# Kernel optimization log

Hardware: AMD Instinct MI355X
Metric: run time of the kernel (lower is better)

Reference implementation:

```python
import jax, jax.numpy as jnp
import numpy as np

B, T, N, H = 512, 128, 256, 256  # batch, time_step, input_size, hidden_size


def setup_inputs() -> dict:
    key = jax.random.key(0)
    ks = jax.random.split(key, 8)
    s_lin = 1.0 / np.sqrt(T)
    s_ih = 1.0 / np.sqrt(H)
    return {
        "X": jax.random.normal(ks[0], (B, T, N), dtype=jnp.float32),
        "Wq": jax.random.uniform(ks[1], (T, T), jnp.float32, -s_lin, s_lin),
        "Wk": jax.random.uniform(ks[2], (T, T), jnp.float32, -s_lin, s_lin),
        "Wv": jax.random.uniform(ks[3], (T, T), jnp.float32, -s_lin, s_lin),
        "W_ih": jax.random.uniform(ks[4], (4 * H, N), jnp.float32, -s_ih, s_ih),
        "W_hh": jax.random.uniform(ks[5], (4 * H, H), jnp.float32, -s_ih, s_ih),
        "b_ih": jax.random.uniform(ks[6], (4 * H,), jnp.float32, -s_ih, s_ih),
        "b_hh": jax.random.uniform(ks[7], (4 * H,), jnp.float32, -s_ih, s_ih),
    }


def _forward(X, Wq, Wk, Wv, W_ih, W_hh, b_ih, b_hh):
    b, t, n = X.shape
    Xp = jnp.swapaxes(X, 1, 2)  # (B, N, T)
    Q = Xp @ Wq.T               # (B, N, T)
    K = Xp @ Wk.T               # (B, N, T)
    V = Xp @ Wv.T               # (B, N, T)
    # QK[b,i,j] = sum_t Q[b,i,t] * K[b,j,t]; scale by sqrt(N)
    scores = jnp.einsum('bit,bjt->bij', Q, K) / jnp.sqrt(jnp.float32(n))
    A = jax.nn.softmax(scores, axis=-1)          # (B, N, N)
    Xa = jnp.einsum('bij,bjt->bit', A, V)        # (B, N, T)
    Xa = jnp.swapaxes(Xa, 1, 2)                  # (B, T, N)

    h0 = jnp.zeros((b, W_hh.shape[1]), X.dtype)
    c0 = h0

    def step(carry, x_t):
        h, c = carry
        gates = x_t @ W_ih.T + b_ih + h @ W_hh.T + b_hh  # (B, 4H)
        i, f, g, o = jnp.split(gates, 4, axis=-1)         # PyTorch gate order
        i = jax.nn.sigmoid(i)
        f = jax.nn.sigmoid(f)
        g = jnp.tanh(g)
        o = jax.nn.sigmoid(o)
        c = f * c + i * g
        h = o * jnp.tanh(c)
        return (h, c), h

    _, hs = jax.lax.scan(step, (h0, c0), jnp.swapaxes(Xa, 0, 1))  # (T, B, H)
    return jnp.swapaxes(hs, 0, 1)  # (B, T, H)


def reference(X, Wq, Wk, Wv, W_ih, W_hh, b_ih, b_hh):
    return _forward(X, Wq, Wk, Wv, W_ih, W_hh, b_ih, b_hh)
```

## Files before the change

### kernel.cpp

```cpp
#include <hip/hip_runtime.h>
#include <hip/hip_bf16.h>
#include <stdint.h>


#define DI __device__ __forceinline__

typedef __attribute__((ext_vector_type(8))) short bf16x8;
typedef __attribute__((ext_vector_type(4))) short short4v;
typedef __attribute__((ext_vector_type(4))) float f32x4;
typedef __attribute__((ext_vector_type(4))) int int4v;

union U8 { bf16x8 v; short4v h[2]; int4v i; };

DI unsigned short f2bf(float x){
  union { float f; unsigned u; } v; v.f = x;
  unsigned r = v.u + 0x7fffu + ((v.u >> 16) & 1u);
  return (unsigned short)(r >> 16);
}
DI float bf2f(unsigned short x){
  union { unsigned u; float f; } v; v.u = ((unsigned)x) << 16; return v.f;
}
DI float rcp_(float x){ return __builtin_amdgcn_rcpf(x); }
DI float sigm(float x){ return rcp_(1.0f + __expf(-x)); }
DI float tanhf_(float x){ return 1.0f - 2.0f * rcp_(1.0f + __expf(2.0f * x)); }

#define BB 512
#define TT 128
#define NN 256
#define HH 256

__global__ void k_prep(const float* __restrict__ Wq, const float* __restrict__ Wk,
                       const float* __restrict__ Wv,
                       const float* __restrict__ bih, const float* __restrict__ bhh,
                       unsigned short* __restrict__ wqb, unsigned short* __restrict__ wkb,
                       unsigned short* __restrict__ wvb,
                       float* __restrict__ bias, int* __restrict__ flags){
  int i = blockIdx.x * 256 + threadIdx.x;
  if (i < 16384){ wqb[i] = f2bf(Wq[i]); wkb[i] = f2bf(Wk[i]); wvb[i] = f2bf(Wv[i]); }
  if (i < 1024){ bias[i] = bih[i] + bhh[i]; }
  if (i < 256){ flags[i] = 0; }
}

__global__ void k_prep2(const float* __restrict__ W, unsigned short* __restrict__ w_f){
  int idx = blockIdx.x * 256 + threadIdx.x;
  int j = idx >> 3, kk = idx & 7;
  const float* src = W + j * 256 + kk * 32;
  unsigned short o[32];
  #pragma unroll
  for (int g = 0; g < 4; ++g)
    #pragma unroll
    for (int e = 0; e < 4; ++e){
      o[g * 8 + e]     = f2bf(src[4 * g + e]);
      o[g * 8 + 4 + e] = f2bf(src[16 + 4 * g + e]);
    }
  int4v* dst = (int4v*)((char*)w_f + j * 512 + kk * 64);
  #pragma unroll
  for (int q = 0; q < 4; ++q) dst[q] = *(int4v*)(o + q * 8);
}

__global__ __launch_bounds__(256) void k_qkv2(const float* __restrict__ X,
      const unsigned short* __restrict__ Wqb, const unsigned short* __restrict__ Wkb,
      const unsigned short* __restrict__ Wvb,
      unsigned short* __restrict__ Qo, unsigned short* __restrict__ Ko,
      unsigned short* __restrict__ Vo){
  __shared__ __align__(16) char smem[98816];
  char* As2 = smem;
  float* tile = (float*)(smem + 32768);
  char* Bs = smem + 32768;
  char* Os = smem + 65536;
  int bid = blockIdx.x;
  int b = bid >> 1, nh = bid & 1;
  int n0 = nh * 128;
  int m0 = b * 256 + n0;
  int tid = threadIdx.x;

  {
    int nl = tid & 127, tg = tid >> 7;
    const float* src = X + (size_t)b * TT * NN + n0 + nl;
    #pragma unroll
    for (int r = 0; r < 64; ++r){
      int t = r * 2 + tg;
      tile[t * 129 + nl] = src[(size_t)t * NN];
    }
  }
  __syncthreads();
  {
    int tpos = tid & 31, nrow = tid >> 5;
    #pragma unroll
    for (int rr = 0; rr < 16; ++rr){
      int n = rr * 8 + nrow;
      int t0 = tpos * 4;
      short4v v = { (short)f2bf(tile[(t0    ) * 129 + n]),
                    (short)f2bf(tile[(t0 + 1) * 129 + n]),
                    (short)f2bf(tile[(t0 + 2) * 129 + n]),
                    (short)f2bf(tile[(t0 + 3) * 129 + n]) };
      *(short4v*)(As2 + n * 256 + ((t0 * 2) ^ ((n & 7) << 4))) = v;
    }
  }

  int lane = tid & 63, wv = tid >> 6;
  int wr = wv >> 1, wc = wv & 1;
  int l15 = lane & 15, g = lane >> 4;
  f32x4 zro = {0.f, 0.f, 0.f, 0.f};

  #pragma unroll 1
  for (int mode = 0; mode < 3; ++mode){
    const unsigned short* W = (mode == 0) ? Wqb : ((mode == 1) ? Wkb : Wvb);
    __syncthreads();
    #pragma unroll
    for (int it = 0; it < 16; ++it){
      int c = it * 256 + tid;
      int j = c >> 5;
      int kc = (c & 31) << 2;
      short4v v = *(const short4v*)(W + j * 128 + kc);
      *(short4v*)(Bs + j * 256 + ((kc * 2) ^ ((j & 7) << 4))) = v;
    }
    __syncthreads();
    f32x4 acc[4][4];
    #pragma unroll
    for (int a = 0; a < 4; ++a)
      #pragma unroll
      for (int bq = 0; bq < 4; ++bq) acc[a][bq] = zro;
    #pragma unroll
    for (int ks = 0; ks < 4; ++ks){
      U8 af[4];
      #pragma unroll
      for (int mt = 0; mt < 4; ++mt){
        int ar = wr * 64 + mt * 16 + l15;
        const char* ab = As2 + ar * 256;
        int sw = (ar & 7) << 4;
        af[mt].h[0] = *(const short4v*)(ab + ((ks * 64 + 8 * g) ^ sw));
        af[mt].h[1] = *(const short4v*)(ab + ((ks * 64 + 8 * g + 32) ^ sw));
      }
      #pragma unroll
      for (int nt = 0; nt < 4; ++nt){
        int jr = wc * 64 + nt * 16 + l15;
        const char* bb = Bs + jr * 256;
        int kb = ks * 64 + 8 * g, sw = (jr & 7) << 4;
        U8 bf;
        bf.h[0] = *(const short4v*)(bb + (kb ^ sw));
        bf.h[1] = *(const short4v*)(bb + ((kb + 32) ^ sw));
        #pragma unroll
        for (int mt = 0; mt < 4; ++mt)
          acc[mt][nt] = __builtin_amdgcn_mfma_f32_16x16x32_bf16(af[mt].v, bf.v, acc[mt][nt], 0, 0, 0);
      }
    }
    float scale = (mode == 0) ? 0.0625f : 1.0f;
    #pragma unroll
    for (int mt = 0; mt < 4; ++mt)
      #pragma unroll
      for (int nt = 0; nt < 4; ++nt)
        #pragma unroll
        for (int r = 0; r < 4; ++r){
          int row = wr * 64 + mt * 16 + g * 4 + r;
          int col = wc * 64 + nt * 16 + l15;
          unsigned short hv = f2bf(acc[mt][nt][r] * scale);
          int addr = (mode == 2) ? (col * 256 + ((row * 2) ^ ((col & 7) << 4)))
                                 : (row * 256 + ((col * 2) ^ ((row & 7) << 4)));
          *(unsigned short*)(Os + addr) = hv;
        }
    __syncthreads();
    int orow = tid >> 1, oseg = tid & 1;
    const char* srcrow = Os + orow * 256;
    unsigned short* dst;
    if (mode == 2){
      dst = Vo + ((size_t)b * 128 + orow) * 256 + n0 + oseg * 64;
    } else {
      dst = ((mode == 0) ? Qo : Ko) + (size_t)(m0 + orow) * 128 + oseg * 64;
    }
    #pragma unroll
    for (int c = 0; c < 8; ++c){
      int kb = oseg * 128 + c * 16;
      *(int4v*)((char*)dst + c * 16) = *(const int4v*)(srcrow + (kb ^ ((orow & 7) << 4)));
    }
  }
}

__global__ __launch_bounds__(512) void k_attn2(const unsigned short* __restrict__ Q,
        const unsigned short* __restrict__ K, const unsigned short* __restrict__ Vt,
        unsigned short* __restrict__ Xa){
  __shared__ __align__(16) char smem[131072 + 512];
  char* Qs = smem;
  char* Ks = smem + 32768;
  char* Ps = smem;
  char* Vs = smem + 65536;
  float* rden = (float*)(smem + 131072);
  int b = blockIdx.y, i0 = blockIdx.x * 128;
  int tid = threadIdx.x, lane = tid & 63, wv = tid >> 6;
  int l15 = lane & 15, g = lane >> 4;

  {
    int row = tid >> 2, q = tid & 3;
    const char* src = (const char*)(Q + ((size_t)b * 256 + i0 + row) * 128) + q * 64;
    char* dstr = Qs + row * 256;
    int sw = (row & 7) << 4;
    #pragma unroll
    for (int c = 0; c < 4; ++c){
      int kb = q * 64 + c * 16;
      *(int4v*)(dstr + (kb ^ sw)) = *(const int4v*)(src + c * 16);
    }
  }
  {
    int row = tid >> 1, half = tid & 1;
    const char* src = (const char*)(K + ((size_t)b * 256 + row) * 128) + half * 128;
    char* dstr = Ks + row * 256;
    int sw = (row & 7) << 4;
    #pragma unroll
    for (int c = 0; c < 8; ++c){
      int kb = half * 128 + c * 16;
      *(int4v*)(dstr + (kb ^ sw)) = *(const int4v*)(src + c * 16);
    }
  }
  __syncthreads();

  f32x4 zro = {0.f, 0.f, 0.f, 0.f};
  f32x4 acc[16];
  #pragma unroll
  for (int nt = 0; nt < 16; ++nt) acc[nt] = zro;
  #pragma unroll
  for (int kk = 0; kk < 4; ++kk){
    int ar = wv * 16 + l15;
    const char* ab = Qs + ar * 256;
    int kb = kk * 64 + 8 * g, swa = (ar & 7) << 4;
    U8 a;
    a.h[0] = *(const short4v*)(ab + (kb ^ swa));
    a.h[1] = *(const short4v*)(ab + ((kb + 32) ^ swa));
    #pragma unroll
    for (int nt = 0; nt < 16; ++nt){
      int jr = nt * 16 + l15;
      const char* bb = Ks + jr * 256;
      int swb = (jr & 7) << 4;
      U8 bf;
      bf.h[0] = *(const short4v*)(bb + (kb ^ swb));
      bf.h[1] = *(const short4v*)(bb + ((kb + 32) ^ swb));
      acc[nt] = __builtin_amdgcn_mfma_f32_16x16x32_bf16(a.v, bf.v, acc[nt], 0, 0, 0);
    }
  }
  float mx[4], sm[4];
  #pragma unroll
  for (int r = 0; r < 4; ++r){
    float m = acc[0][r];
    #pragma unroll
    for (int nt = 1; nt < 16; ++nt) m = fmaxf(m, acc[nt][r]);
    #pragma unroll
    for (int s = 1; s < 16; s <<= 1) m = fmaxf(m, __shfl_xor(m, s));
    mx[r] = m;
  }
  #pragma unroll
  for (int r = 0; r < 4; ++r){
    float s = 0.f;
    #pragma unroll
    for (int nt = 0; nt < 16; ++nt){
      float p = __expf(acc[nt][r] - mx[r]);
      acc[nt][r] = p; s += p;
    }
    #pragma unroll
    for (int sd = 1; sd < 16; sd <<= 1) s += __shfl_xor(s, sd);
    sm[r] = s;
  }
  __syncthreads();
  #pragma unroll
  for (int nt = 0; nt < 16; ++nt)
    #pragma unroll
    for (int r = 0; r < 4; ++r){
      int ir = wv * 16 + g * 4 + r;
      *(unsigned short*)(Ps + ir * 512 + ((nt * 16 + l15) * 2 ^ ((ir & 7) << 4))) = f2bf(acc[nt][r]);
    }
  #pragma unroll
  for (int r = 0; r < 4; ++r)
    if (l15 == r) rden[wv * 16 + g * 4 + r] = rcp_(sm[r]);
  {
    int row = tid >> 2, q = tid & 3;
    const char* src = (const char*)(Vt + ((size_t)b * 128 + row) * 256) + q * 128;
    char* dstr = Vs + row * 512;
    int sw = (row & 7) << 4;
    #pragma unroll
    for (int c = 0; c < 8; ++c){
      int jb = q * 128 + c * 16;
      *(int4v*)(dstr + (jb ^ sw)) = *(const int4v*)(src + c * 16);
    }
  }
  __syncthreads();

  f32x4 acc2[8];
  #pragma unroll
  for (int nt = 0; nt < 8; ++nt) acc2[nt] = zro;
  #pragma unroll
  for (int kk = 0; kk < 8; ++kk){
    int kb = kk * 64 + 8 * g;
    U8 bfr[8];
    #pragma unroll
    for (int nt = 0; nt < 8; ++nt){
      int ir = nt * 16 + l15;
      const char* pb = Ps + ir * 512;
      int sw = (ir & 7) << 4;
      bfr[nt].h[0] = *(const short4v*)(pb + (kb ^ sw));
      bfr[nt].h[1] = *(const short4v*)(pb + ((kb + 32) ^ sw));
    }
    int tr = wv * 16 + l15;
    const char* ab = Vs + tr * 512;
    int sw = (tr & 7) << 4;
    U8 a;
    a.h[0] = *(const short4v*)(ab + (kb ^ sw));
    a.h[1] = *(const short4v*)(ab + ((kb + 32) ^ sw));
    #pragma unroll
    for (int nt = 0; nt < 8; ++nt)
      acc2[nt] = __builtin_amdgcn_mfma_f32_16x16x32_bf16(a.v, bfr[nt].v, acc2[nt], 0, 0, 0);
  }
  #pragma unroll
  for (int nt = 0; nt < 8; ++nt){
    float rd = rden[nt * 16 + l15];
    #pragma unroll
    for (int r = 0; r < 4; ++r){
      int t = wv * 16 + g * 4 + r;
      int i = i0 + nt * 16 + l15;
      Xa[((size_t)b * 128 + t) * 256 + i] = f2bf(acc2[nt][r] * rd);
    }
  }
}

__global__ __launch_bounds__(512, 2) void k_lstm8(const unsigned short* __restrict__ Xa,
        const unsigned short* __restrict__ whh_f, const unsigned short* __restrict__ wih_f,
        const float* __restrict__ bias, float* __restrict__ out,
        unsigned int* __restrict__ hbuf, int* __restrict__ flags){
  __shared__ __align__(16) char smem[131072 + 8192 + 8192 + 8448];
  char* WI = smem;
  char* HS = smem + 131072;
  char* XS = smem + 139264;
  float* GS = (float*)(smem + 147456);
  int tid = threadIdx.x, lane = tid & 63, wv = tid >> 6;
  int l15 = lane & 15, g = lane >> 4;
  int bid = blockIdx.x;
  int x = bid & 7, q = bid >> 3;
  int y = q >> 2, m = q & 3;
  int grp = y * 8 + x;
  int b0 = grp * 8;
  int c0 = m * 64;
  int tb = tid >> 6, tc = tid & 63;

  U8 breg[2][8];
  #pragma unroll
  for (int nt = 0; nt < 2; ++nt){
    int jl = wv * 32 + nt * 16 + l15;
    int jg = (jl >> 6) * 256 + c0 + (jl & 63);
    #pragma unroll
    for (int kk = 0; kk < 8; ++kk)
      breg[nt][kk].i = *(const int4v*)((const char*)whh_f + (size_t)jg * 512 + kk * 64 + g * 16);
  }
  {
    int jl = tid >> 1, hq = (tid & 1) * 16;
    int jg = (jl >> 6) * 256 + c0 + (jl & 63);
    const char* src = (const char*)wih_f + (size_t)jg * 512;
    char* dst = WI + jl * 512;
    int sx = jl & 7;
    #pragma unroll
    for (int c2 = 0; c2 < 16; ++c2){
      int c = hq + c2;
      *(int4v*)(dst + ((c ^ sx) << 4)) = *(const int4v*)(src + c * 16);
    }
  }
  { int4v z = {0,0,0,0}; *(int4v*)(HS + tid * 16) = z; }
  if (tid < 256){ int4v z = {0,0,0,0}; *(int4v*)(XS + 4096 + tid * 16) = z; }
  {
    short4v v = *(const short4v*)(Xa + ((size_t)(b0 + tb) * 128) * 256 + tc * 4);
    *(short4v*)(XS + tb * 512 + ((tc * 8) ^ ((tb & 7) << 3))) = v;
  }
  float bs0 = bias[      c0 + tc], bs1 = bias[256 + c0 + tc];
  float bs2 = bias[512 + c0 + tc], bs3 = bias[768 + c0 + tc];
  float cst = 0.f;
  __syncthreads();

  int swA = (l15 & 7) << 3;
  const char* hsrow = HS + l15 * 512;
  const char* xsrow = XS + l15 * 512;
  const char* wib0 = WI + (wv * 32 + l15) * 512;
  const char* wib1 = WI + (wv * 32 + 16 + l15) * 512;
  int keep = g >> 1;
  f32x4 zro = {0.f, 0.f, 0.f, 0.f};

  f32x4 accX[2] = {zro, zro};
  #pragma unroll
  for (int kk = 0; kk < 8; ++kk){
    U8 a2, w0, w1;
    a2.h[0] = *(const short4v*)(xsrow + ((kk * 64 + 8 * g) ^ swA));
    a2.h[1] = *(const short4v*)(xsrow + ((kk * 64 + 32 + 8 * g) ^ swA));
    int cx = ((kk * 4 + g) ^ (l15 & 7)) << 4;
    w0.i = *(const int4v*)(wib0 + cx);
    w1.i = *(const int4v*)(wib1 + cx);
    accX[0] = __builtin_amdgcn_mfma_f32_16x16x32_bf16(a2.v, w0.v, accX[0], 0, 0, 0);
    accX[1] = __builtin_amdgcn_mfma_f32_16x16x32_bf16(a2.v, w1.v, accX[1], 0, 0, 0);
  }

  #pragma unroll 1
  for (int t = 0; t < 128; ++t){
    short4v xan = {0, 0, 0, 0};
    if (t < 127)
      xan = *(const short4v*)(Xa + ((size_t)(b0 + tb) * 128 + (t + 1)) * 256 + tc * 4);
    f32x4 acc[2] = {accX[0], accX[1]};
    #pragma unroll
    for (int kk = 0; kk < 8; ++kk){
      U8 a;
      a.h[0] = *(const short4v*)(hsrow + ((kk * 64 + 8 * g) ^ swA));
      a.h[1] = *(const short4v*)(hsrow + ((kk * 64 + 32 + 8 * g) ^ swA));
      acc[0] = __builtin_amdgcn_mfma_f32_16x16x32_bf16(a.v, breg[0][kk].v, acc[0], 0, 0, 0);
      acc[1] = __builtin_amdgcn_mfma_f32_16x16x32_bf16(a.v, breg[1][kk].v, acc[1], 0, 0, 0);
    }
    #pragma unroll
    for (int r = 0; r < 4; ++r){
      float v0 = acc[0][r], v1 = acc[1][r];
      float kv = keep ? v1 : v0;
      float sv = keep ? v0 : v1;
      float val = kv + __shfl_xor(sv, 32);
      int jl = wv * 32 + keep * 16 + l15;
      int batch = (g & 1) * 4 + r;
      GS[batch * 264 + (jl >> 6) * 66 + (jl & 63)] = val;
    }
    __syncthreads();
    float gv0 = GS[tb * 264 +   0 + tc];
    float gv1 = GS[tb * 264 +  66 + tc];
    float gv2 = GS[tb * 264 + 132 + tc];
    float gv3 = GS[tb * 264 + 198 + tc];
    float gi = sigm(gv0 + bs0);
    float gf = sigm(gv1 + bs1);
    float gg = tanhf_(gv2 + bs2);
    float go = sigm(gv3 + bs3);
    float c = gf * cst + gi * gg;
    cst = c;
    float h = go * tanhf_(c);
    out[((size_t)(b0 + tb) * 128 + t) * 256 + c0 + tc] = h;
    if (t < 127){
      unsigned short hhi = f2bf(h);
      unsigned short hlo = f2bf(h - bf2f(hhi));
      unsigned int pk = (unsigned int)hhi | ((unsigned int)hlo << 16);
      unsigned int* hb = hbuf + ((size_t)grp * 2 + (t & 1)) * 2048;
      __hip_atomic_store(hb + tb * 256 + c0 + tc, pk, __ATOMIC_RELAXED, __HIP_MEMORY_SCOPE_SYSTEM);
      *(short4v*)(XS + tb * 512 + ((tc * 8) ^ ((tb & 7) << 3))) = xan;
      __syncthreads();
      if (wv == 0 && lane == 0)
        __hip_atomic_store(&flags[grp * 4 + m], t + 1, __ATOMIC_RELAXED, __HIP_MEMORY_SCOPE_SYSTEM);
      accX[0] = zro; accX[1] = zro;
      #pragma unroll
      for (int kk = 0; kk < 8; ++kk){
        U8 a2, w0, w1;
        a2.h[0] = *(const short4v*)(xsrow + ((kk * 64 + 8 * g) ^ swA));
        a2.h[1] = *(const short4v*)(xsrow + ((kk * 64 + 32 + 8 * g) ^ swA));
        int cx = ((kk * 4 + g) ^ (l15 & 7)) << 4;
        w0.i = *(const int4v*)(wib0 + cx);
        w1.i = *(const int4v*)(wib1 + cx);
        accX[0] = __builtin_amdgcn_mfma_f32_16x16x32_bf16(a2.v, w0.v, accX[0], 0, 0, 0);
        accX[1] = __builtin_amdgcn_mfma_f32_16x16x32_bf16(a2.v, w1.v, accX[1], 0, 0, 0);
      }
      if (wv == 0 && lane >= 1 && lane <= 3){
        int pl = lane - 1;
        int pslot = pl + (pl >= m ? 1 : 0);
        while (__hip_atomic_load(&flags[grp * 4 + pslot], __ATOMIC_RELAXED,
                                 __HIP_MEMORY_SCOPE_SYSTEM) <= t){}
      }
      __syncthreads();
      {
        int bb = tid >> 6, cg = tid & 63;
        const unsigned long long* sp =
            (const unsigned long long*)(hb + bb * 256 + cg * 4);
        unsigned long long w0 = __hip_atomic_load(sp,     __ATOMIC_RELAXED, __HIP_MEMORY_SCOPE_SYSTEM);
        unsigned long long w1 = __hip_atomic_load(sp + 1, __ATOMIC_RELAXED, __HIP_MEMORY_SCOPE_SYSTEM);
        unsigned int u0 = (unsigned int)w0, u1 = (unsigned int)(w0 >> 32);
        unsigned int u2 = (unsigned int)w1, u3 = (unsigned int)(w1 >> 32);
        short4v hiv = { (short)(u0 & 0xffff), (short)(u1 & 0xffff),
                        (short)(u2 & 0xffff), (short)(u3 & 0xffff) };
        short4v lov = { (short)(u0 >> 16), (short)(u1 >> 16),
                        (short)(u2 >> 16), (short)(u3 >> 16) };
        int sw = (bb & 7) << 3;
        int cb = (cg * 8) ^ sw;
        *(short4v*)(HS + bb * 512 + cb) = hiv;
        *(short4v*)(HS + (bb + 8) * 512 + cb) = lov;
      }
      __syncthreads();
    }
  }
}

extern "C" void kernel_launch(void* const* d_in, const int* in_sizes, int n_in,
                              void* d_out, int out_size, void* d_ws, size_t ws_size,
                              hipStream_t stream){
  (void)in_sizes; (void)n_in; (void)out_size; (void)ws_size;
  const float* X   = (const float*)d_in[0];
  const float* Wq  = (const float*)d_in[1];
  const float* Wk  = (const float*)d_in[2];
  const float* Wv  = (const float*)d_in[3];
  const float* Wih = (const float*)d_in[4];
  const float* Whh = (const float*)d_in[5];
  const float* bih = (const float*)d_in[6];
  const float* bhh = (const float*)d_in[7];
  float* out = (float*)d_out;
  char* ws = (char*)d_ws;

  const size_t SZ = 33554432ULL;
  unsigned short* p_q  = (unsigned short*)ws;
  unsigned short* p_k  = (unsigned short*)(ws + SZ);
  unsigned short* p_vt = (unsigned short*)(ws + 2 * SZ);
  unsigned short* p_xa = (unsigned short*)(ws + 3 * SZ);
  char* p = ws + 4 * SZ;
  unsigned short* p_wqb = (unsigned short*)p; p += 32768;
  unsigned short* p_wkb = (unsigned short*)p; p += 32768;
  unsigned short* p_wvb = (unsigned short*)p; p += 32768;
  unsigned short* p_whhf= (unsigned short*)p; p += 524288;
  unsigned short* p_wihf= (unsigned short*)p; p += 524288;
  float* p_bias = (float*)p; p += 4096;
  unsigned int* p_hbuf = (unsigned int*)p; p += 1048576;
  int* p_flags = (int*)p;

  k_prep<<<64, 256, 0, stream>>>(Wq, Wk, Wv, bih, bhh,
                                 p_wqb, p_wkb, p_wvb, p_bias, p_flags);
  k_prep2<<<32, 256, 0, stream>>>(Whh, p_whhf);
  k_prep2<<<32, 256, 0, stream>>>(Wih, p_wihf);
  k_qkv2<<<1024, 256, 0, stream>>>(X, p_wqb, p_wkb, p_wvb, p_q, p_k, p_vt);
  k_attn2<<<dim3(2, 512), 512, 0, stream>>>(p_q, p_k, p_vt, p_xa);
  k_lstm8<<<256, 512, 0, stream>>>(p_xa, p_whhf, p_wihf, p_bias, out, p_hbuf, p_flags);
}
```

Baseline: 525.7 us.

## Merge prep kernels, narrow atomic scope to agent, drop barrier in LSTM spin-wait

The three weight-prep kernels become one launch, saving two launch gaps. The LSTM's cross-block h-exchange atomics and flags move from system scope to agent scope, which can avoid system-coherent memory traffic. Every wave now spins on the peer flags itself, and the block-wide barrier after the wait is removed, shortening the per-step critical path. There is a correctness risk: each wave relies on its own spin before reading hbuf, with only relaxed ordering on the flag load.

```diff
diff --git a/kernel.cpp b/kernel.cpp
--- a/kernel.cpp
+++ b/kernel.cpp
@@ -29,20 +29,25 @@
 #define NN 256
 #define HH 256
 
-__global__ void k_prep(const float* __restrict__ Wq, const float* __restrict__ Wk,
-                       const float* __restrict__ Wv,
-                       const float* __restrict__ bih, const float* __restrict__ bhh,
-                       unsigned short* __restrict__ wqb, unsigned short* __restrict__ wkb,
-                       unsigned short* __restrict__ wvb,
-                       float* __restrict__ bias, int* __restrict__ flags){
-  int i = blockIdx.x * 256 + threadIdx.x;
-  if (i < 16384){ wqb[i] = f2bf(Wq[i]); wkb[i] = f2bf(Wk[i]); wvb[i] = f2bf(Wv[i]); }
-  if (i < 1024){ bias[i] = bih[i] + bhh[i]; }
-  if (i < 256){ flags[i] = 0; }
-}
-
-__global__ void k_prep2(const float* __restrict__ W, unsigned short* __restrict__ w_f){
-  int idx = blockIdx.x * 256 + threadIdx.x;
+__global__ void k_prep3(const float* __restrict__ Wq, const float* __restrict__ Wk,
+                        const float* __restrict__ Wv, const float* __restrict__ Wih,
+                        const float* __restrict__ Whh,
+                        const float* __restrict__ bih, const float* __restrict__ bhh,
+                        unsigned short* __restrict__ wqb, unsigned short* __restrict__ wkb,
+                        unsigned short* __restrict__ wvb,
+                        unsigned short* __restrict__ wihf, unsigned short* __restrict__ whhf,
+                        float* __restrict__ bias, int* __restrict__ flags){
+  int bx = blockIdx.x;
+  if (bx < 64){
+    int i = bx * 256 + threadIdx.x;
+    wqb[i] = f2bf(Wq[i]); wkb[i] = f2bf(Wk[i]); wvb[i] = f2bf(Wv[i]);
+    if (i < 1024) bias[i] = bih[i] + bhh[i];
+    if (i < 256) flags[i] = 0;
+    return;
+  }
+  const float* W = (bx < 96) ? Whh : Wih;
+  unsigned short* w_f = (bx < 96) ? whhf : wihf;
+  int idx = ((bx < 96) ? (bx - 64) : (bx - 96)) * 256 + threadIdx.x;
   int j = idx >> 3, kk = idx & 7;
   const float* src = W + j * 256 + kk * 32;
   unsigned short o[32];
@@ -319,7 +324,7 @@
   }
 }
 
-__global__ __launch_bounds__(512, 2) void k_lstm8(const unsigned short* __restrict__ Xa,
+__global__ __launch_bounds__(512, 2) void k_lstm9(const unsigned short* __restrict__ Xa,
         const unsigned short* __restrict__ whh_f, const unsigned short* __restrict__ wih_f,
         const float* __restrict__ bias, float* __restrict__ out,
         unsigned int* __restrict__ hbuf, int* __restrict__ flags){
@@ -433,11 +438,11 @@
       unsigned short hlo = f2bf(h - bf2f(hhi));
       unsigned int pk = (unsigned int)hhi | ((unsigned int)hlo << 16);
       unsigned int* hb = hbuf + ((size_t)grp * 2 + (t & 1)) * 2048;
-      __hip_atomic_store(hb + tb * 256 + c0 + tc, pk, __ATOMIC_RELAXED, __HIP_MEMORY_SCOPE_SYSTEM);
+      __hip_atomic_store(hb + tb * 256 + c0 + tc, pk, __ATOMIC_RELAXED, __HIP_MEMORY_SCOPE_AGENT);
       *(short4v*)(XS + tb * 512 + ((tc * 8) ^ ((tb & 7) << 3))) = xan;
       __syncthreads();
-      if (wv == 0 && lane == 0)
-        __hip_atomic_store(&flags[grp * 4 + m], t + 1, __ATOMIC_RELAXED, __HIP_MEMORY_SCOPE_SYSTEM);
+      if (tid == 0)
+        __hip_atomic_store(&flags[grp * 4 + m], t + 1, __ATOMIC_RELAXED, __HIP_MEMORY_SCOPE_AGENT);
       accX[0] = zro; accX[1] = zro;
       #pragma unroll
       for (int kk = 0; kk < 8; ++kk){
@@ -450,19 +455,18 @@
         accX[0] = __builtin_amdgcn_mfma_f32_16x16x32_bf16(a2.v, w0.v, accX[0], 0, 0, 0);
         accX[1] = __builtin_amdgcn_mfma_f32_16x16x32_bf16(a2.v, w1.v, accX[1], 0, 0, 0);
       }
-      if (wv == 0 && lane >= 1 && lane <= 3){
+      if (lane >= 1 && lane <= 3){
         int pl = lane - 1;
         int pslot = pl + (pl >= m ? 1 : 0);
         while (__hip_atomic_load(&flags[grp * 4 + pslot], __ATOMIC_RELAXED,
-                                 __HIP_MEMORY_SCOPE_SYSTEM) <= t){}
+                                 __HIP_MEMORY_SCOPE_AGENT) <= t){}
       }
-      __syncthreads();
       {
         int bb = tid >> 6, cg = tid & 63;
         const unsigned long long* sp =
             (const unsigned long long*)(hb + bb * 256 + cg * 4);
-        unsigned long long w0 = __hip_atomic_load(sp,     __ATOMIC_RELAXED, __HIP_MEMORY_SCOPE_SYSTEM);
-        unsigned long long w1 = __hip_atomic_load(sp + 1, __ATOMIC_RELAXED, __HIP_MEMORY_SCOPE_SYSTEM);
+        unsigned long long w0 = __hip_atomic_load(sp,     __ATOMIC_RELAXED, __HIP_MEMORY_SCOPE_AGENT);
+        unsigned long long w1 = __hip_atomic_load(sp + 1, __ATOMIC_RELAXED, __HIP_MEMORY_SCOPE_AGENT);
         unsigned int u0 = (unsigned int)w0, u1 = (unsigned int)(w0 >> 32);
         unsigned int u2 = (unsigned int)w1, u3 = (unsigned int)(w1 >> 32);
         short4v hiv = { (short)(u0 & 0xffff), (short)(u1 & 0xffff),
@@ -509,11 +513,10 @@
   unsigned int* p_hbuf = (unsigned int*)p; p += 1048576;
   int* p_flags = (int*)p;
 
-  k_prep<<<64, 256, 0, stream>>>(Wq, Wk, Wv, bih, bhh,
-                                 p_wqb, p_wkb, p_wvb, p_bias, p_flags);
-  k_prep2<<<32, 256, 0, stream>>>(Whh, p_whhf);
-  k_prep2<<<32, 256, 0, stream>>>(Wih, p_wihf);
+  k_prep3<<<128, 256, 0, stream>>>(Wq, Wk, Wv, Wih, Whh, bih, bhh,
+                                   p_wqb, p_wkb, p_wvb, p_wihf, p_whhf,
+                                   p_bias, p_flags);
   k_qkv2<<<1024, 256, 0, stream>>>(X, p_wqb, p_wkb, p_wvb, p_q, p_k, p_vt);
   k_attn2<<<dim3(2, 512), 512, 0, stream>>>(p_q, p_k, p_vt, p_xa);
-  k_lstm8<<<256, 512, 0, stream>>>(p_xa, p_whhf, p_wihf, p_bias, out, p_hbuf, p_flags);
-}
+  k_lstm9<<<256, 512, 0, stream>>>(p_xa, p_whhf, p_wihf, p_bias, out, p_hbuf, p_flags);
+}
```

After: 514.4 us. 2.1% less time.
